# Kernel optimization log

Measured on AMD Instinct MI355X. Metric: run time of the kernel, lower is better.

The kernel has to match this reference:

```python
import jax, jax.numpy as jnp
import numpy as np

N_NODES = 100000
N_EDGES = 1600000


def setup_inputs() -> dict:
    key = jax.random.key(0)
    k1, k2, k3, k4 = jax.random.split(key, 4)
    x = jax.random.normal(k1, (N_NODES, 256), dtype=jnp.float32)
    edge_index = jax.random.randint(k2, (2, N_EDGES), 0, N_NODES, dtype=jnp.int64)
    W1 = jax.random.normal(k3, (256, 128), dtype=jnp.float32) * (1.0 / np.sqrt(256))
    W2 = jax.random.normal(k4, (128, 40), dtype=jnp.float32) * (1.0 / np.sqrt(128))
    return {"x": x, "edge_index": edge_index, "W1": W1, "W2": W2}


def _gcn_conv(x, W, src, dst):
    # GCNConv(normalize=False, add_self_loops=False, bias=False):
    # linear transform then sum-aggregate messages along edges src->dst.
    h = x @ W                                   # [N, d_out]
    msg = h[src]                                # [E, d_out] gather
    return jax.ops.segment_sum(msg, dst, num_segments=N_NODES)  # [N, d_out] scatter-add


def reference(x, edge_index, W1, W2):
    src, dst = edge_index[0], edge_index[1]
    h = jax.nn.relu(_gcn_conv(x, W1, src, dst))
    # dropout is identity in eval mode
    out = _gcn_conv(h, W2, src, dst)
    return out
```

## Files before the change

kernel.cpp:

```cpp
#include <hip/hip_runtime.h>

constexpr int NN = 100000;
constexpr int NE = 1600000;
constexpr int DI = 256, DH = 128, DO = 40;

constexpr int NB = (NN + 255) >> 8;
constexpr int NB_BLK = 128;
constexpr int CHUNK = NE / NB_BLK;
constexpr int M2 = NB * NB_BLK;
constexpr int NBS = (M2 + 1023) / 1024;
constexpr int STAGE_CAP = 6144;

typedef __attribute__((ext_vector_type(8))) __bf16 bf16x8;
typedef __attribute__((ext_vector_type(4))) float f32x4;

__device__ inline float4 bf4_to_f4(ushort4 u) {
    return make_float4(__builtin_bit_cast(float, (unsigned)u.x << 16),
                       __builtin_bit_cast(float, (unsigned)u.y << 16),
                       __builtin_bit_cast(float, (unsigned)u.z << 16),
                       __builtin_bit_cast(float, (unsigned)u.w << 16));
}
__device__ inline unsigned short f2bf(float f) {
    return __builtin_bit_cast(unsigned short, (__bf16)f);
}
__device__ inline bf16x8 bf16x8_zero() {
    bf16x8 r;
    #pragma unroll
    for (int j = 0; j < 8; ++j) r[j] = (__bf16)0.f;
    return r;
}
__device__ inline bf16x8 load_cvt_a(const float* __restrict__ p, bool ok) {
    if (!ok) return bf16x8_zero();
    bf16x8 r;
    const float4 v0 = *(const float4*)p;
    const float4 v1 = *(const float4*)(p + 4);
    r[0] = (__bf16)v0.x; r[1] = (__bf16)v0.y; r[2] = (__bf16)v0.z; r[3] = (__bf16)v0.w;
    r[4] = (__bf16)v1.x; r[5] = (__bf16)v1.y; r[6] = (__bf16)v1.z; r[7] = (__bf16)v1.w;
    return r;
}
__device__ inline void acc4(float4& a, float4 v) {
    a.x += v.x; a.y += v.y; a.z += v.z; a.w += v.w;
}

__global__ __launch_bounds__(256) void wpack_kernel(const float* __restrict__ W1,
                                                    const float* __restrict__ W2,
                                                    __bf16* __restrict__ Wf,
                                                    __bf16* __restrict__ Wf2) {
    if (blockIdx.x < 128) {
        const int i = blockIdx.x * 256 + threadIdx.x;
        const int j = i & 7;
        const int lane = (i >> 3) & 63;
        const int nt = (i >> 9) & 7;
        const int kt = i >> 12;
        const int k = kt * 32 + (lane >> 4) * 8 + j;
        const int n = nt * 16 + (lane & 15);
        Wf[i] = (__bf16)W1[(size_t)k * DH + n];
    } else {
        const int i = (blockIdx.x - 128) * 256 + threadIdx.x;
        if (i < 6144) {
            const int j = i & 7;
            const int lane = (i >> 3) & 63;
            const int g = i >> 9;
            const int nt = g % 3, ks = g / 3;
            const int k = ks * 32 + (lane >> 4) * 8 + j;
            const int n = nt * 16 + (lane & 15);
            Wf2[i] = (n < DO) ? (__bf16)W2[(size_t)k * DO + n] : (__bf16)0.f;
        }
    }
}

__global__ __launch_bounds__(256) void gemm1_kernel(const float* __restrict__ x,
                                                    const __bf16* __restrict__ Wf,
                                                    __bf16* __restrict__ h1) {
    const int t = threadIdx.x;
    const int wave = t >> 6, lane = t & 63;
    const int q = lane >> 4, m = lane & 15;
    const int row0 = blockIdx.x * 64 + wave * 16;
    const int r = row0 + m;
    const bool ok = r < NN;
    const float* xp = x + (size_t)r * DI;

    bf16x8 a[8];
    #pragma unroll
    for (int kt = 0; kt < 8; ++kt)
        a[kt] = load_cvt_a(xp + kt * 32 + q * 8, ok);

    f32x4 acc[8];
    #pragma unroll
    for (int nt = 0; nt < 8; ++nt)
        #pragma unroll
        for (int rr = 0; rr < 4; ++rr) acc[nt][rr] = 0.f;

    const bf16x8* wf = (const bf16x8*)Wf;
    #pragma unroll
    for (int kt = 0; kt < 8; ++kt) {
        #pragma unroll
        for (int nt = 0; nt < 8; ++nt) {
            const bf16x8 b = wf[(kt * 8 + nt) * 64 + lane];
            acc[nt] = __builtin_amdgcn_mfma_f32_16x16x32_bf16(a[kt], b, acc[nt], 0, 0, 0);
        }
    }
    #pragma unroll
    for (int reg = 0; reg < 4; ++reg) {
        const int rr = row0 + q * 4 + reg;
        if (rr < NN) {
            __bf16* hp = h1 + (size_t)rr * DH + m;
            #pragma unroll
            for (int nt = 0; nt < 8; ++nt) hp[nt * 16] = (__bf16)acc[nt][reg];
        }
    }
}

__global__ __launch_bounds__(256) void bucket_hist_kernel(const int* __restrict__ dst,
                                                          int* __restrict__ hist2d) {
    __shared__ int h[NB];
    for (int i = threadIdx.x; i < NB; i += 256) h[i] = 0;
    __syncthreads();
    const int base = blockIdx.x * CHUNK;
    for (int i = threadIdx.x; i < CHUNK; i += 256)
        atomicAdd(&h[dst[base + i] >> 8], 1);
    __syncthreads();
    for (int i = threadIdx.x; i < NB; i += 256)
        hist2d[i * NB_BLK + blockIdx.x] = h[i];
}

__global__ __launch_bounds__(256) void spart_kernel(const int* __restrict__ in,
                                                    int* __restrict__ bsum) {
    __shared__ int red[256];
    const int idx = blockIdx.x * 1024 + threadIdx.x * 4;
    int s = 0;
    if (idx < M2) { const int4 v = *(const int4*)(in + idx); s = v.x + v.y + v.z + v.w; }
    red[threadIdx.x] = s;
    __syncthreads();
    #pragma unroll
    for (int d = 128; d > 0; d >>= 1) {
        if (threadIdx.x < d) red[threadIdx.x] += red[threadIdx.x + d];
        __syncthreads();
    }
    if (threadIdx.x == 0) bsum[blockIdx.x] = red[0];
}

__global__ __launch_bounds__(64) void sblock_kernel(const int* __restrict__ bsum,
                                                    int* __restrict__ boff) {
    __shared__ int part[64];
    const int t = threadIdx.x;
    const int v = (t < NBS) ? bsum[t] : 0;
    part[t] = v;
    __syncthreads();
    for (int d = 1; d < 64; d <<= 1) {
        const int u = (t >= d) ? part[t - d] : 0;
        __syncthreads();
        part[t] += u;
        __syncthreads();
    }
    if (t < NBS) boff[t] = part[t] - v;
}

__global__ __launch_bounds__(256) void sfinal_kernel(const int* __restrict__ in,
                                                     const int* __restrict__ boff,
                                                     int* __restrict__ out) {
    __shared__ int part[256];
    const int t = threadIdx.x;
    const int idx = blockIdx.x * 1024 + t * 4;
    int4 v = make_int4(0, 0, 0, 0);
    if (idx < M2) v = *(const int4*)(in + idx);
    const int s = v.x + v.y + v.z + v.w;
    part[t] = s;
    __syncthreads();
    for (int d = 1; d < 256; d <<= 1) {
        const int u = (t >= d) ? part[t - d] : 0;
        __syncthreads();
        part[t] += u;
        __syncthreads();
    }
    if (idx < M2) {
        const int base = boff[blockIdx.x] + part[t] - s;
        *(int4*)(out + idx) = make_int4(base, base + v.x, base + v.x + v.y,
                                        base + v.x + v.y + v.z);
    }
}

__global__ __launch_bounds__(256) void bucket_scatter_kernel(const int* __restrict__ src,
                                                             const int* __restrict__ dst,
                                                             const int* __restrict__ offs2d,
                                                             unsigned* __restrict__ epack) {
    __shared__ int cur[NB];
    for (int i = threadIdx.x; i < NB; i += 256)
        cur[i] = offs2d[i * NB_BLK + blockIdx.x];
    __syncthreads();
    const int base = blockIdx.x * CHUNK;
    for (int i = threadIdx.x; i < CHUNK; i += 256) {
        const int d = dst[base + i], s = src[base + i];
        const int p = atomicAdd(&cur[d >> 8], 1);
        epack[p] = (unsigned)s | ((unsigned)(d & 255) << 24);
    }
}

__global__ __launch_bounds__(256) void bucket_sort_kernel(const unsigned* __restrict__ epack,
                                                          const int* __restrict__ offs2d,
                                                          int* __restrict__ off,
                                                          int* __restrict__ esrc) {
    __shared__ int cnt[256];
    __shared__ int incl[256];
    __shared__ int cur[256];
    __shared__ int stage[STAGE_CAP];
    const int b = blockIdx.x;
    const int t = threadIdx.x;
    const int bstart = offs2d[b * NB_BLK];
    const int bend = (b + 1 < NB) ? offs2d[(b + 1) * NB_BLK] : NE;
    const int n = bend - bstart;
    cnt[t] = 0;
    __syncthreads();
    for (int i = t; i < n; i += 256)
        atomicAdd(&cnt[epack[bstart + i] >> 24], 1);
    __syncthreads();
    incl[t] = cnt[t];
    __syncthreads();
    for (int d = 1; d < 256; d <<= 1) {
        const int u = (t >= d) ? incl[t - d] : 0;
        __syncthreads();
        incl[t] += u;
        __syncthreads();
    }
    const int ex = incl[t] - cnt[t];
    const int node = (b << 8) + t;
    if (node <= NN) off[node] = bstart + ex;
    cur[t] = ex;
    __syncthreads();
    const bool staged = (n <= STAGE_CAP);
    for (int i = t; i < n; i += 256) {
        const unsigned pk = epack[bstart + i];
        const int p = atomicAdd(&cur[pk >> 24], 1);
        const int s = (int)(pk & 0xFFFFFFu);
        if (staged) stage[p] = s;
        else esrc[bstart + p] = s;
    }
    __syncthreads();
    if (staged)
        for (int i = t; i < n; i += 256) esrc[bstart + i] = stage[i];
}

__global__ __launch_bounds__(256) void agg1_kernel(const __bf16* __restrict__ h1,
                                                   const int* __restrict__ esrc,
                                                   const int* __restrict__ off,
                                                   __bf16* __restrict__ agg) {
    const int w = (blockIdx.x * 256 + threadIdx.x) >> 6;
    if (w >= NN) return;
    const int lane = threadIdx.x & 63;
    const int half = lane >> 5;
    const int c = (lane & 31) * 4;
    const int b = off[w], e = off[w + 1];
    const int deg = e - b;
    float4 a0 = make_float4(0.f, 0.f, 0.f, 0.f);
    float4 a1 = a0, a2 = a0, a3 = a0, a4 = a0, a5 = a0, a6 = a0, a7 = a0;

    for (int base = 0; base < deg; base += 64) {
        const int cnt = min(64, deg - base);
        const int cl = cnt - 1;
        const int idx = (base + lane < deg) ? esrc[b + base + lane] : 0;
        int kk = 0;
        for (; kk + 16 <= cnt; kk += 16) {
            const int s0 = __shfl(idx, kk + half);
            const int s1 = __shfl(idx, kk + 2 + half);
            const int s2 = __shfl(idx, kk + 4 + half);
            const int s3 = __shfl(idx, kk + 6 + half);
            const int s4 = __shfl(idx, kk + 8 + half);
            const int s5 = __shfl(idx, kk + 10 + half);
            const int s6 = __shfl(idx, kk + 12 + half);
            const int s7 = __shfl(idx, kk + 14 + half);
            acc4(a0, bf4_to_f4(*(const ushort4*)(h1 + (size_t)s0 * DH + c)));
            acc4(a1, bf4_to_f4(*(const ushort4*)(h1 + (size_t)s1 * DH + c)));
            acc4(a2, bf4_to_f4(*(const ushort4*)(h1 + (size_t)s2 * DH + c)));
            acc4(a3, bf4_to_f4(*(const ushort4*)(h1 + (size_t)s3 * DH + c)));
            acc4(a4, bf4_to_f4(*(const ushort4*)(h1 + (size_t)s4 * DH + c)));
            acc4(a5, bf4_to_f4(*(const ushort4*)(h1 + (size_t)s5 * DH + c)));
            acc4(a6, bf4_to_f4(*(const ushort4*)(h1 + (size_t)s6 * DH + c)));
            acc4(a7, bf4_to_f4(*(const ushort4*)(h1 + (size_t)s7 * DH + c)));
        }
        for (; kk + 8 <= cnt; kk += 8) {
            const int s0 = __shfl(idx, kk + half);
            const int s1 = __shfl(idx, kk + 2 + half);
            const int s2 = __shfl(idx, kk + 4 + half);
            const int s3 = __shfl(idx, kk + 6 + half);
            acc4(a0, bf4_to_f4(*(const ushort4*)(h1 + (size_t)s0 * DH + c)));
            acc4(a1, bf4_to_f4(*(const ushort4*)(h1 + (size_t)s1 * DH + c)));
            acc4(a2, bf4_to_f4(*(const ushort4*)(h1 + (size_t)s2 * DH + c)));
            acc4(a3, bf4_to_f4(*(const ushort4*)(h1 + (size_t)s3 * DH + c)));
        }
        for (; kk < cnt; kk += 2) {
            const int ei = kk + half;
            const int s0 = __shfl(idx, (ei < cnt) ? ei : cl);
            const float4 v = bf4_to_f4(*(const ushort4*)(h1 + (size_t)s0 * DH + c));
            if (ei < cnt) acc4(a0, v);
        }
    }
    float4 acc = make_float4(a0.x + a1.x + a2.x + a3.x + a4.x + a5.x + a6.x + a7.x,
                             a0.y + a1.y + a2.y + a3.y + a4.y + a5.y + a6.y + a7.y,
                             a0.z + a1.z + a2.z + a3.z + a4.z + a5.z + a6.z + a7.z,
                             a0.w + a1.w + a2.w + a3.w + a4.w + a5.w + a6.w + a7.w);
    acc.x += __shfl_xor(acc.x, 32);
    acc.y += __shfl_xor(acc.y, 32);
    acc.z += __shfl_xor(acc.z, 32);
    acc.w += __shfl_xor(acc.w, 32);
    if (half == 0) {
        ushort4 o;
        o.x = f2bf(fmaxf(acc.x, 0.f));
        o.y = f2bf(fmaxf(acc.y, 0.f));
        o.z = f2bf(fmaxf(acc.z, 0.f));
        o.w = f2bf(fmaxf(acc.w, 0.f));
        *(ushort4*)(agg + (size_t)w * DH + c) = o;
    }
}

__global__ __launch_bounds__(256) void gemm2_kernel(const __bf16* __restrict__ agg,
                                                    const __bf16* __restrict__ Wf2,
                                                    __bf16* __restrict__ h2) {
    const int t = threadIdx.x;
    const int wave = t >> 6, lane = t & 63;
    const int q = lane >> 4, m = lane & 15;
    const int row0 = blockIdx.x * 64 + wave * 16;
    const int r = row0 + m;
    const bool ok = r < NN;
    const __bf16* ap = agg + (size_t)r * DH;

    f32x4 acc[3];
    #pragma unroll
    for (int nt = 0; nt < 3; ++nt)
        #pragma unroll
        for (int rr = 0; rr < 4; ++rr) acc[nt][rr] = 0.f;

    const bf16x8* wf2 = (const bf16x8*)Wf2;
    #pragma unroll
    for (int ks = 0; ks < 4; ++ks) {
        const int k0 = ks * 32 + q * 8;
        const bf16x8 a = ok ? *(const bf16x8*)(ap + k0) : bf16x8_zero();
        #pragma unroll
        for (int nt = 0; nt < 3; ++nt) {
            const bf16x8 b = wf2[(ks * 3 + nt) * 64 + lane];
            acc[nt] = __builtin_amdgcn_mfma_f32_16x16x32_bf16(a, b, acc[nt], 0, 0, 0);
        }
    }
    #pragma unroll
    for (int reg = 0; reg < 4; ++reg) {
        const int rr = row0 + q * 4 + reg;
        if (rr < NN) {
            #pragma unroll
            for (int nt = 0; nt < 3; ++nt) {
                const int cc = nt * 16 + m;
                if (cc < DO) h2[(size_t)rr * DO + cc] = (__bf16)acc[nt][reg];
            }
        }
    }
}

__global__ __launch_bounds__(256) void agg2_kernel(const __bf16* __restrict__ h2,
                                                   const int* __restrict__ esrc,
                                                   const int* __restrict__ off,
                                                   float* __restrict__ out) {
    const int w = (blockIdx.x * 256 + threadIdx.x) >> 6;
    if (w >= NN) return;
    const int lane = threadIdx.x & 63;
    const int sub = lane / 10;
    const int c = (lane % 10) * 4;
    const int b = off[w], e = off[w + 1];
    const int deg = e - b;
    float4 a0 = make_float4(0.f, 0.f, 0.f, 0.f);
    float4 a1 = a0, a2 = a0, a3 = a0;

    for (int base = 0; base < deg; base += 64) {
        const int cnt = min(64, deg - base);
        const int cl = cnt - 1;
        const int idx = (base + lane < deg) ? esrc[b + base + lane] : 0;
        const bool act = sub < 6;
        int kk = 0;
        for (; kk + 24 <= cnt; kk += 24) {
            const int e0 = kk + sub;
            const int s0 = __shfl(idx, min(e0, cl));
            const int s1 = __shfl(idx, min(e0 + 6, cl));
            const int s2 = __shfl(idx, min(e0 + 12, cl));
            const int s3 = __shfl(idx, min(e0 + 18, cl));
            const float4 v0 = bf4_to_f4(*(const ushort4*)(h2 + (size_t)s0 * DO + c));
            const float4 v1 = bf4_to_f4(*(const ushort4*)(h2 + (size_t)s1 * DO + c));
            const float4 v2 = bf4_to_f4(*(const ushort4*)(h2 + (size_t)s2 * DO + c));
            const float4 v3 = bf4_to_f4(*(const ushort4*)(h2 + (size_t)s3 * DO + c));
            if (act) { acc4(a0, v0); acc4(a1, v1); acc4(a2, v2); acc4(a3, v3); }
        }
        for (; kk + 12 <= cnt; kk += 12) {
            const int e0 = kk + sub;
            const int s0 = __shfl(idx, min(e0, cl));
            const int s1 = __shfl(idx, min(e0 + 6, cl));
            const float4 v0 = bf4_to_f4(*(const ushort4*)(h2 + (size_t)s0 * DO + c));
            const float4 v1 = bf4_to_f4(*(const ushort4*)(h2 + (size_t)s1 * DO + c));
            if (act) { acc4(a0, v0); acc4(a1, v1); }
        }
        for (; kk < cnt; kk += 6) {
            const int e0 = kk + sub;
            const int s0 = __shfl(idx, min(e0, cl));
            const float4 v = bf4_to_f4(*(const ushort4*)(h2 + (size_t)s0 * DO + c));
            if (act && e0 < cnt) acc4(a0, v);
        }
    }
    float4 acc = make_float4(a0.x + a1.x + a2.x + a3.x, a0.y + a1.y + a2.y + a3.y,
                             a0.z + a1.z + a2.z + a3.z, a0.w + a1.w + a2.w + a3.w);
    acc.x += __shfl(acc.x, lane + 30);
    acc.y += __shfl(acc.y, lane + 30);
    acc.z += __shfl(acc.z, lane + 30);
    acc.w += __shfl(acc.w, lane + 30);
    const float ax = acc.x + __shfl(acc.x, lane + 10) + __shfl(acc.x, lane + 20);
    const float ay = acc.y + __shfl(acc.y, lane + 10) + __shfl(acc.y, lane + 20);
    const float az = acc.z + __shfl(acc.z, lane + 10) + __shfl(acc.z, lane + 20);
    const float aw = acc.w + __shfl(acc.w, lane + 10) + __shfl(acc.w, lane + 20);
    if (lane < 10) {
        *(float4*)(out + (size_t)w * DO + c) = make_float4(ax, ay, az, aw);
    }
}

extern "C" void kernel_launch(void* const* d_in, const int* in_sizes, int n_in,
                              void* d_out, int out_size, void* d_ws, size_t ws_size,
                              hipStream_t stream) {
    const float* x  = (const float*)d_in[0];
    const int*   ei = (const int*)d_in[1];
    const float* W1 = (const float*)d_in[2];
    const float* W2 = (const float*)d_in[3];
    const int* src = ei;
    const int* dst = ei + NE;

    __bf16* Wf  = (__bf16*)d_ws;
    __bf16* Wf2 = Wf + 32768;
    __bf16* h1  = Wf2 + 6144;
    __bf16* agg = h1 + (size_t)NN * DH;
    __bf16* h2  = h1;
    unsigned* epack = (unsigned*)(agg + (size_t)NN * DH);
    int* esrc   = (int*)(epack + NE);
    int* off    = esrc + NE;
    int* hist2d = off + NN + 1;
    int* offs2d = hist2d + M2;
    int* bsum   = offs2d + M2;
    int* boff   = bsum + NBS;

    float* out = (float*)d_out;

    wpack_kernel<<<152, 256, 0, stream>>>(W1, W2, Wf, Wf2);
    gemm1_kernel<<<(NN + 63) / 64, 256, 0, stream>>>(x, Wf, h1);
    bucket_hist_kernel<<<NB_BLK, 256, 0, stream>>>(dst, hist2d);
    spart_kernel<<<NBS, 256, 0, stream>>>(hist2d, bsum);
    sblock_kernel<<<1, 64, 0, stream>>>(bsum, boff);
    sfinal_kernel<<<NBS, 256, 0, stream>>>(hist2d, boff, offs2d);
    bucket_scatter_kernel<<<NB_BLK, 256, 0, stream>>>(src, dst, offs2d, epack);
    bucket_sort_kernel<<<NB, 256, 0, stream>>>(epack, offs2d, off, esrc);
    agg1_kernel<<<(NN * 64 + 255) / 256, 256, 0, stream>>>(h1, esrc, off, agg);
    gemm2_kernel<<<(NN + 63) / 64, 256, 0, stream>>>(agg, Wf2, h2);
    agg2_kernel<<<(NN * 64 + 255) / 256, 256, 0, stream>>>(h2, esrc, off, out);
}
```

Before: 366.9 us.

## Merge wpack with histogram, gemm1 with scan, and simplify agg1 gather loop

Folds the bucket histogram into the weight-pack launch and the three-kernel prefix scan into the gemm1 launch as extra blocks. Each scan block recomputes its own base by reducing all preceding histogram entries, replacing the separate block-sum passes. This cuts six launches to two and lets independent work overlap. The agg1 kernel also drops the wave-wide index load and shuffle scheme for direct per-lane esrc loads with 4-way unrolling, which trades shuffles for redundant index loads and fewer accumulators.

```diff
diff --git a/kernel.cpp b/kernel.cpp
--- a/kernel.cpp
+++ b/kernel.cpp
@@ -10,6 +10,8 @@
 constexpr int M2 = NB * NB_BLK;
 constexpr int NBS = (M2 + 1023) / 1024;
 constexpr int STAGE_CAP = 6144;
+constexpr int WPACK_BLOCKS = 152;
+constexpr int GEMM1_BLOCKS = (NN + 63) / 64;
 
 typedef __attribute__((ext_vector_type(8))) __bf16 bf16x8;
 typedef __attribute__((ext_vector_type(4))) float f32x4;
@@ -42,10 +44,13 @@
     a.x += v.x; a.y += v.y; a.z += v.z; a.w += v.w;
 }
 
-__global__ __launch_bounds__(256) void wpack_kernel(const float* __restrict__ W1,
-                                                    const float* __restrict__ W2,
-                                                    __bf16* __restrict__ Wf,
-                                                    __bf16* __restrict__ Wf2) {
+__global__ __launch_bounds__(256) void wpack_hist_kernel(const float* __restrict__ W1,
+                                                         const float* __restrict__ W2,
+                                                         const int* __restrict__ dst,
+                                                         __bf16* __restrict__ Wf,
+                                                         __bf16* __restrict__ Wf2,
+                                                         int* __restrict__ hist2d) {
+    __shared__ int h[NB];
     if (blockIdx.x < 128) {
         const int i = blockIdx.x * 256 + threadIdx.x;
         const int j = i & 7;
@@ -55,7 +60,7 @@
         const int k = kt * 32 + (lane >> 4) * 8 + j;
         const int n = nt * 16 + (lane & 15);
         Wf[i] = (__bf16)W1[(size_t)k * DH + n];
-    } else {
+    } else if (blockIdx.x < WPACK_BLOCKS) {
         const int i = (blockIdx.x - 128) * 256 + threadIdx.x;
         if (i < 6144) {
             const int j = i & 7;
@@ -66,117 +71,98 @@
             const int n = nt * 16 + (lane & 15);
             Wf2[i] = (n < DO) ? (__bf16)W2[(size_t)k * DO + n] : (__bf16)0.f;
         }
-    }
-}
-
-__global__ __launch_bounds__(256) void gemm1_kernel(const float* __restrict__ x,
-                                                    const __bf16* __restrict__ Wf,
-                                                    __bf16* __restrict__ h1) {
-    const int t = threadIdx.x;
-    const int wave = t >> 6, lane = t & 63;
-    const int q = lane >> 4, m = lane & 15;
-    const int row0 = blockIdx.x * 64 + wave * 16;
-    const int r = row0 + m;
-    const bool ok = r < NN;
-    const float* xp = x + (size_t)r * DI;
-
-    bf16x8 a[8];
-    #pragma unroll
-    for (int kt = 0; kt < 8; ++kt)
-        a[kt] = load_cvt_a(xp + kt * 32 + q * 8, ok);
-
-    f32x4 acc[8];
-    #pragma unroll
-    for (int nt = 0; nt < 8; ++nt)
-        #pragma unroll
-        for (int rr = 0; rr < 4; ++rr) acc[nt][rr] = 0.f;
-
-    const bf16x8* wf = (const bf16x8*)Wf;
-    #pragma unroll
-    for (int kt = 0; kt < 8; ++kt) {
-        #pragma unroll
-        for (int nt = 0; nt < 8; ++nt) {
-            const bf16x8 b = wf[(kt * 8 + nt) * 64 + lane];
-            acc[nt] = __builtin_amdgcn_mfma_f32_16x16x32_bf16(a[kt], b, acc[nt], 0, 0, 0);
-        }
-    }
-    #pragma unroll
-    for (int reg = 0; reg < 4; ++reg) {
-        const int rr = row0 + q * 4 + reg;
-        if (rr < NN) {
-            __bf16* hp = h1 + (size_t)rr * DH + m;
+    } else {
+        const int hb = blockIdx.x - WPACK_BLOCKS;
+        for (int i = threadIdx.x; i < NB; i += 256) h[i] = 0;
+        __syncthreads();
+        const int base = hb * CHUNK;
+        for (int i = threadIdx.x; i < CHUNK; i += 256)
+            atomicAdd(&h[dst[base + i] >> 8], 1);
+        __syncthreads();
+        for (int i = threadIdx.x; i < NB; i += 256)
+            hist2d[i * NB_BLK + hb] = h[i];
+    }
+}
+
+__global__ __launch_bounds__(256) void gemm1_scan_kernel(const float* __restrict__ x,
+                                                         const __bf16* __restrict__ Wf,
+                                                         __bf16* __restrict__ h1,
+                                                         const int* __restrict__ hist2d,
+                                                         int* __restrict__ offs2d) {
+    __shared__ int red[256];
+    if (blockIdx.x < GEMM1_BLOCKS) {
+        const int t = threadIdx.x;
+        const int wave = t >> 6, lane = t & 63;
+        const int q = lane >> 4, m = lane & 15;
+        const int row0 = blockIdx.x * 64 + wave * 16;
+        const int r = row0 + m;
+        const bool ok = r < NN;
+        const float* xp = x + (size_t)r * DI;
+
+        bf16x8 a[8];
+        #pragma unroll
+        for (int kt = 0; kt < 8; ++kt)
+            a[kt] = load_cvt_a(xp + kt * 32 + q * 8, ok);
+
+        f32x4 acc[8];
+        #pragma unroll
+        for (int nt = 0; nt < 8; ++nt)
             #pragma unroll
-            for (int nt = 0; nt < 8; ++nt) hp[nt * 16] = (__bf16)acc[nt][reg];
-        }
-    }
-}
-
-__global__ __launch_bounds__(256) void bucket_hist_kernel(const int* __restrict__ dst,
-                                                          int* __restrict__ hist2d) {
-    __shared__ int h[NB];
-    for (int i = threadIdx.x; i < NB; i += 256) h[i] = 0;
-    __syncthreads();
-    const int base = blockIdx.x * CHUNK;
-    for (int i = threadIdx.x; i < CHUNK; i += 256)
-        atomicAdd(&h[dst[base + i] >> 8], 1);
-    __syncthreads();
-    for (int i = threadIdx.x; i < NB; i += 256)
-        hist2d[i * NB_BLK + blockIdx.x] = h[i];
-}
-
-__global__ __launch_bounds__(256) void spart_kernel(const int* __restrict__ in,
-                                                    int* __restrict__ bsum) {
-    __shared__ int red[256];
-    const int idx = blockIdx.x * 1024 + threadIdx.x * 4;
-    int s = 0;
-    if (idx < M2) { const int4 v = *(const int4*)(in + idx); s = v.x + v.y + v.z + v.w; }
-    red[threadIdx.x] = s;
-    __syncthreads();
-    #pragma unroll
-    for (int d = 128; d > 0; d >>= 1) {
-        if (threadIdx.x < d) red[threadIdx.x] += red[threadIdx.x + d];
-        __syncthreads();
-    }
-    if (threadIdx.x == 0) bsum[blockIdx.x] = red[0];
-}
-
-__global__ __launch_bounds__(64) void sblock_kernel(const int* __restrict__ bsum,
-                                                    int* __restrict__ boff) {
-    __shared__ int part[64];
-    const int t = threadIdx.x;
-    const int v = (t < NBS) ? bsum[t] : 0;
-    part[t] = v;
-    __syncthreads();
-    for (int d = 1; d < 64; d <<= 1) {
-        const int u = (t >= d) ? part[t - d] : 0;
-        __syncthreads();
-        part[t] += u;
-        __syncthreads();
-    }
-    if (t < NBS) boff[t] = part[t] - v;
-}
-
-__global__ __launch_bounds__(256) void sfinal_kernel(const int* __restrict__ in,
-                                                     const int* __restrict__ boff,
-                                                     int* __restrict__ out) {
-    __shared__ int part[256];
-    const int t = threadIdx.x;
-    const int idx = blockIdx.x * 1024 + t * 4;
-    int4 v = make_int4(0, 0, 0, 0);
-    if (idx < M2) v = *(const int4*)(in + idx);
-    const int s = v.x + v.y + v.z + v.w;
-    part[t] = s;
-    __syncthreads();
-    for (int d = 1; d < 256; d <<= 1) {
-        const int u = (t >= d) ? part[t - d] : 0;
-        __syncthreads();
-        part[t] += u;
-        __syncthreads();
-    }
-    if (idx < M2) {
-        const int base = boff[blockIdx.x] + part[t] - s;
-        *(int4*)(out + idx) = make_int4(base, base + v.x, base + v.x + v.y,
-                                        base + v.x + v.y + v.z);
+            for (int rr = 0; rr < 4; ++rr) acc[nt][rr] = 0.f;
+
+        const bf16x8* wf = (const bf16x8*)Wf;
+        #pragma unroll
+        for (int kt = 0; kt < 8; ++kt) {
+            #pragma unroll
+            for (int nt = 0; nt < 8; ++nt) {
+                const bf16x8 b = wf[(kt * 8 + nt) * 64 + lane];
+                acc[nt] = __builtin_amdgcn_mfma_f32_16x16x32_bf16(a[kt], b, acc[nt], 0, 0, 0);
+            }
+        }
+        #pragma unroll
+        for (int reg = 0; reg < 4; ++reg) {
+            const int rr = row0 + q * 4 + reg;
+            if (rr < NN) {
+                __bf16* hp = h1 + (size_t)rr * DH + m;
+                #pragma unroll
+                for (int nt = 0; nt < 8; ++nt) hp[nt * 16] = (__bf16)acc[nt][reg];
+            }
+        }
+    } else {
+        const int b = blockIdx.x - GEMM1_BLOCKS;
+        const int t = threadIdx.x;
+        int s = 0;
+        const int limit = b * 1024;
+        for (int i = t * 4; i < limit; i += 1024) {
+            const int4 v = *(const int4*)(hist2d + i);
+            s += v.x + v.y + v.z + v.w;
+        }
+        red[t] = s;
+        __syncthreads();
+        #pragma unroll
+        for (int d = 128; d > 0; d >>= 1) {
+            if (t < d) red[t] += red[t + d];
+            __syncthreads();
+        }
+        const int base = red[0];
+        __syncthreads();
+        const int idx = b * 1024 + t * 4;
+        int4 v = make_int4(0, 0, 0, 0);
+        if (idx < M2) v = *(const int4*)(hist2d + idx);
+        const int sl = v.x + v.y + v.z + v.w;
+        red[t] = sl;
+        __syncthreads();
+        for (int d = 1; d < 256; d <<= 1) {
+            const int u = (t >= d) ? red[t - d] : 0;
+            __syncthreads();
+            red[t] += u;
+            __syncthreads();
+        }
+        if (idx < M2) {
+            const int e0 = base + red[t] - sl;
+            *(int4*)(offs2d + idx) = make_int4(e0, e0 + v.x, e0 + v.x + v.y,
+                                               e0 + v.x + v.y + v.z);
+        }
     }
 }
 
@@ -250,54 +236,24 @@
     const int half = lane >> 5;
     const int c = (lane & 31) * 4;
     const int b = off[w], e = off[w + 1];
-    const int deg = e - b;
     float4 a0 = make_float4(0.f, 0.f, 0.f, 0.f);
-    float4 a1 = a0, a2 = a0, a3 = a0, a4 = a0, a5 = a0, a6 = a0, a7 = a0;
-
-    for (int base = 0; base < deg; base += 64) {
-        const int cnt = min(64, deg - base);
-        const int cl = cnt - 1;
-        const int idx = (base + lane < deg) ? esrc[b + base + lane] : 0;
-        int kk = 0;
-        for (; kk + 16 <= cnt; kk += 16) {
-            const int s0 = __shfl(idx, kk + half);
-            const int s1 = __shfl(idx, kk + 2 + half);
-            const int s2 = __shfl(idx, kk + 4 + half);
-            const int s3 = __shfl(idx, kk + 6 + half);
-            const int s4 = __shfl(idx, kk + 8 + half);
-            const int s5 = __shfl(idx, kk + 10 + half);
-            const int s6 = __shfl(idx, kk + 12 + half);
-            const int s7 = __shfl(idx, kk + 14 + half);
-            acc4(a0, bf4_to_f4(*(const ushort4*)(h1 + (size_t)s0 * DH + c)));
-            acc4(a1, bf4_to_f4(*(const ushort4*)(h1 + (size_t)s1 * DH + c)));
-            acc4(a2, bf4_to_f4(*(const ushort4*)(h1 + (size_t)s2 * DH + c)));
-            acc4(a3, bf4_to_f4(*(const ushort4*)(h1 + (size_t)s3 * DH + c)));
-            acc4(a4, bf4_to_f4(*(const ushort4*)(h1 + (size_t)s4 * DH + c)));
-            acc4(a5, bf4_to_f4(*(const ushort4*)(h1 + (size_t)s5 * DH + c)));
-            acc4(a6, bf4_to_f4(*(const ushort4*)(h1 + (size_t)s6 * DH + c)));
-            acc4(a7, bf4_to_f4(*(const ushort4*)(h1 + (size_t)s7 * DH + c)));
-        }
-        for (; kk + 8 <= cnt; kk += 8) {
-            const int s0 = __shfl(idx, kk + half);
-            const int s1 = __shfl(idx, kk + 2 + half);
-            const int s2 = __shfl(idx, kk + 4 + half);
-            const int s3 = __shfl(idx, kk + 6 + half);
-            acc4(a0, bf4_to_f4(*(const ushort4*)(h1 + (size_t)s0 * DH + c)));
-            acc4(a1, bf4_to_f4(*(const ushort4*)(h1 + (size_t)s1 * DH + c)));
-            acc4(a2, bf4_to_f4(*(const ushort4*)(h1 + (size_t)s2 * DH + c)));
-            acc4(a3, bf4_to_f4(*(const ushort4*)(h1 + (size_t)s3 * DH + c)));
-        }
-        for (; kk < cnt; kk += 2) {
-            const int ei = kk + half;
-            const int s0 = __shfl(idx, (ei < cnt) ? ei : cl);
-            const float4 v = bf4_to_f4(*(const ushort4*)(h1 + (size_t)s0 * DH + c));
-            if (ei < cnt) acc4(a0, v);
-        }
-    }
-    float4 acc = make_float4(a0.x + a1.x + a2.x + a3.x + a4.x + a5.x + a6.x + a7.x,
-                             a0.y + a1.y + a2.y + a3.y + a4.y + a5.y + a6.y + a7.y,
-                             a0.z + a1.z + a2.z + a3.z + a4.z + a5.z + a6.z + a7.z,
-                             a0.w + a1.w + a2.w + a3.w + a4.w + a5.w + a6.w + a7.w);
+    float4 a1 = a0, a2 = a0, a3 = a0;
+    int j = b + half;
+    for (; j + 6 < e; j += 8) {
+        const int s0 = esrc[j], s1 = esrc[j + 2], s2 = esrc[j + 4], s3 = esrc[j + 6];
+        acc4(a0, bf4_to_f4(*(const ushort4*)(h1 + (size_t)s0 * DH + c)));
+        acc4(a1, bf4_to_f4(*(const ushort4*)(h1 + (size_t)s1 * DH + c)));
+        acc4(a2, bf4_to_f4(*(const ushort4*)(h1 + (size_t)s2 * DH + c)));
+        acc4(a3, bf4_to_f4(*(const ushort4*)(h1 + (size_t)s3 * DH + c)));
+    }
+    for (; j < e; j += 2) {
+        const int s = esrc[j];
+        acc4(a0, bf4_to_f4(*(const ushort4*)(h1 + (size_t)s * DH + c)));
+    }
+    float4 acc = make_float4(a0.x + a1.x + a2.x + a3.x,
+                             a0.y + a1.y + a2.y + a3.y,
+                             a0.z + a1.z + a2.z + a3.z,
+                             a0.w + a1.w + a2.w + a3.w);
     acc.x += __shfl_xor(acc.x, 32);
     acc.y += __shfl_xor(acc.y, 32);
     acc.z += __shfl_xor(acc.z, 32);
@@ -435,17 +391,11 @@
     int* off    = esrc + NE;
     int* hist2d = off + NN + 1;
     int* offs2d = hist2d + M2;
-    int* bsum   = offs2d + M2;
-    int* boff   = bsum + NBS;
 
     float* out = (float*)d_out;
 
-    wpack_kernel<<<152, 256, 0, stream>>>(W1, W2, Wf, Wf2);
-    gemm1_kernel<<<(NN + 63) / 64, 256, 0, stream>>>(x, Wf, h1);
-    bucket_hist_kernel<<<NB_BLK, 256, 0, stream>>>(dst, hist2d);
-    spart_kernel<<<NBS, 256, 0, stream>>>(hist2d, bsum);
-    sblock_kernel<<<1, 64, 0, stream>>>(bsum, boff);
-    sfinal_kernel<<<NBS, 256, 0, stream>>>(hist2d, boff, offs2d);
+    wpack_hist_kernel<<<WPACK_BLOCKS + NB_BLK, 256, 0, stream>>>(W1, W2, dst, Wf, Wf2, hist2d);
+    gemm1_scan_kernel<<<GEMM1_BLOCKS + NBS, 256, 0, stream>>>(x, Wf, h1, hist2d, offs2d);
     bucket_scatter_kernel<<<NB_BLK, 256, 0, stream>>>(src, dst, offs2d, epack);
     bucket_sort_kernel<<<NB, 256, 0, stream>>>(epack, offs2d, off, esrc);
     agg1_kernel<<<(NN * 64 + 255) / 256, 256, 0, stream>>>(h1, esrc, off, agg);
```

Result: faster. 354.8 us (-3.3%).
